# Kernel optimization log

Measured on AMD Instinct MI355X. Metric: run time of the kernel, lower is better.

Reference implementation:

```python
import itertools
import jax, jax.numpy as jnp
import numpy as np

GAMMA = 1.0

def setup_inputs() -> dict:
    key = jax.random.key(0)
    ks = jax.random.split(key, 11)
    B, T, NP, NG, J, H = 16, 32, 8, 4, 14, 256
    return {
        'hor_heatmap': jax.random.normal(ks[0], (B, T, 1, H, H), jnp.float32),
        'hor_offset': jax.random.normal(ks[1], (B, T, NP, 2), jnp.float32),
        'hor_bsize': jax.random.normal(ks[2], (B, T, NP, 4), jnp.float32),
        'hor_center': jax.random.normal(ks[3], (B, T, NP, 2), jnp.float32),
        'scores': jax.random.uniform(ks[4], (B, T, NP), jnp.float32),
        'x_pose3d': jax.random.normal(ks[5], (B, T, NP, J, 3), jnp.float32),
        'gt_heatmap': jax.random.normal(ks[6], (B, T, H, H), jnp.float32),
        'gt_hor_boxes_wh': jax.random.normal(ks[7], (B, T, NG, 4), jnp.float32),
        'gt_hor_offset': jax.random.normal(ks[8], (B, T, NG, 2), jnp.float32),
        'gt_hor_center': jax.random.normal(ks[9], (B, T, NG, 2), jnp.float32),
        'gt_pose3d': jax.random.normal(ks[10], (B, T, NG, J, 3), jnp.float32),
    }

def _make_perms(num_pred, num_gt):
    # all injective assignments of each gt column to a distinct pred row
    return np.asarray(list(itertools.permutations(range(num_pred), num_gt)), dtype=np.int32)

def _match(cost, perms):
    # cost: [NP, NG]; perms: [P, NG] static. Exact linear_sum_assignment by enumeration.
    ng = cost.shape[1]
    totals = cost[perms, jnp.arange(ng)].sum(-1)  # [P]
    return perms[jnp.argmin(totals)]              # rows matched to cols 0..NG-1

def reference(hor_heatmap, hor_offset, hor_bsize, hor_center, scores, x_pose3d,
              gt_heatmap, gt_hor_boxes_wh, gt_hor_offset, gt_hor_center, gt_pose3d):
    B, T, NP, _ = hor_center.shape
    NG = gt_hor_center.shape[2]
    J = x_pose3d.shape[3]
    BT = B * T
    perms = jnp.asarray(_make_perms(NP, NG))

    # center loss: MSE mean over full heatmaps
    center_loss = jnp.mean((hor_heatmap[:, :, 0] - gt_heatmap) ** 2)

    # --- Hungarian box/offset losses, vmapped over (b,t) ---
    def per_bt_box(pc, gc, sc, po, go, ps, gs):
        # cost[i,j] = -score[i] + ||pc_i - gc_j||
        C = jnp.linalg.norm(pc[:, None] - gc[None], axis=-1) - sc[:, None]  # [NP,NG]
        rows = _match(C, perms)                                             # [NG]
        off = jnp.mean(jnp.abs(po[rows] - go), axis=-1).sum()   # L1 mean per pair, summed
        size = jnp.mean(jnp.abs(ps[rows] - gs), axis=-1).sum()
        return off, size

    flat = lambda x: x.reshape((BT,) + x.shape[2:])
    offs, sizes = jax.vmap(per_bt_box)(
        flat(hor_center), flat(gt_hor_center), flat(scores),
        flat(hor_offset), flat(gt_hor_offset), flat(hor_bsize), flat(gt_hor_boxes_wh))
    total_offset_loss = offs.sum() / BT
    total_size_loss = sizes.sum() / BT

    # --- Hungarian pose loss ---
    def per_bt_pose(pp, gp):
        d = pp[:, None] - gp[None]                       # [NP,NG,J,3]
        C = jnp.sqrt(jnp.sum(d * d, axis=(-1, -2)))      # Frobenius norm cost
        rows = _match(C, perms)
        return jnp.sum((pp[rows] - gp) ** 2)             # MSE(sum) per pair, summed

    pose_loss = jax.vmap(per_bt_pose)(flat(x_pose3d), flat(gt_pose3d)).sum() / (BT * NP * J)

    detection_loss = center_loss + total_offset_loss + total_size_loss
    return GAMMA * detection_loss + pose_loss
```

## Files before the change

kernel.cpp:

```cpp
#include <hip/hip_runtime.h>

#define BT      512
#define NP      8
#define NG      4
#define JNT     14
#define NCENTER 33554432
#define N4      8388608
#define CBLK    1024
#define CSTEP   (CBLK*256)
#define HALF4   (N4/2)


__global__ __launch_bounds__(256) void center_kernel(
    const float* __restrict__ hm, const float* __restrict__ gt_hm,
    float* __restrict__ ws, int use_atomics)
{
    __shared__ float sv[4];
    const int tid = threadIdx.x;
    const int base = blockIdx.x * 256 + tid;
    const float4* a = (const float4*)hm;
    const float4* b = (const float4*)gt_hm;
    float s0 = 0.0f, s1 = 0.0f;
    for (int k = 0; k < 16; k++) {
        const int i = base + k * CSTEP;
        float4 x0 = a[i];
        float4 y0 = b[i];
        float4 x1 = a[i + HALF4];
        float4 y1 = b[i + HALF4];
        float d0 = x0.x - y0.x, d1 = x0.y - y0.y, d2 = x0.z - y0.z, d3 = x0.w - y0.w;
        s0 += d0 * d0 + d1 * d1 + d2 * d2 + d3 * d3;
        float e0 = x1.x - y1.x, e1 = x1.y - y1.y, e2 = x1.z - y1.z, e3 = x1.w - y1.w;
        s1 += e0 * e0 + e1 * e1 + e2 * e2 + e3 * e3;
    }
    float s = s0 + s1;
    #pragma unroll
    for (int o = 32; o > 0; o >>= 1) s += __shfl_down(s, o);
    const int lane = tid & 63, w = tid >> 6;
    if (lane == 0) sv[w] = s;
    __syncthreads();
    if (tid == 0) {
        float tot = sv[0] + sv[1] + sv[2] + sv[3];
        if (use_atomics) atomicAdd(&ws[0], tot);
        else             ws[blockIdx.x] = tot;
    }
}

__global__ __launch_bounds__(256) void hungarian_kernel(
    const float* __restrict__ hor_offset,
    const float* __restrict__ hor_bsize,
    const float* __restrict__ hor_center,
    const float* __restrict__ scores,
    const float* __restrict__ x_pose3d,
    const float* __restrict__ gt_wh,
    const float* __restrict__ gt_off,
    const float* __restrict__ gt_center,
    const float* __restrict__ gt_pose,
    float* __restrict__ ws, int use_atomics)
{
    __shared__ float sPP[NP * JNT * 3];
    __shared__ float sGP[NG * JNT * 3];
    __shared__ float sPO[NP * 2];
    __shared__ float sGO[NG * 2];
    __shared__ float sPS[NP * 4];
    __shared__ float sGS[NG * 4];
    __shared__ float sPC[NP * 2];
    __shared__ float sGC[NG * 2];
    __shared__ float sSC[NP];
    __shared__ float2 sCC[NP * NG];
    __shared__ float sv[8];
    __shared__ int   spx[8];
    __shared__ int   sBest[2];

    const int c   = blockIdx.x;
    const int tid = threadIdx.x;

    {
        const float* pp = x_pose3d  + c * (NP * JNT * 3);
        const float* gp = gt_pose   + c * (NG * JNT * 3);
        for (int k = tid; k < NP * JNT * 3; k += 256) sPP[k] = pp[k];
        if (tid < NG * JNT * 3) sGP[tid] = gp[tid];
        if (tid < NP * 2) sPO[tid] = hor_offset[c * NP * 2 + tid];
        if (tid < NG * 2) sGO[tid] = gt_off[c * NG * 2 + tid];
        if (tid < NP * 4) sPS[tid] = hor_bsize[c * NP * 4 + tid];
        if (tid < NG * 4) sGS[tid] = gt_wh[c * NG * 4 + tid];
        if (tid < NP * 2) sPC[tid] = hor_center[c * NP * 2 + tid];
        if (tid < NG * 2) sGC[tid] = gt_center[c * NG * 2 + tid];
        if (tid < NP)     sSC[tid] = scores[c * NP + tid];
    }
    __syncthreads();

    if (tid < 32) {
        const int i = tid >> 2, j = tid & 3;
        float dx = sPC[i * 2 + 0] - sGC[j * 2 + 0];
        float dy = sPC[i * 2 + 1] - sGC[j * 2 + 1];
        float box = sqrtf(dx * dx + dy * dy) - sSC[i];
        float acc = 0.0f;
        #pragma unroll
        for (int k = 0; k < JNT * 3; k++) {
            float d = sPP[i * (JNT * 3) + k] - sGP[j * (JNT * 3) + k];
            acc += d * d;
        }
        sCC[i * 4 + j] = make_float2(box, sqrtf(acc));
    }
    __syncthreads();

    float bv = 1e30f, bv2 = 1e30f;
    int bp = 0x7fffffff, bp2 = 0x7fffffff;
    for (int p = tid; p < 4096; p += 256) {
        const int i0 = (p >> 9) & 7, i1 = (p >> 6) & 7, i2 = (p >> 3) & 7, i3 = p & 7;
        if (i0 == i1 || i0 == i2 || i0 == i3 || i1 == i2 || i1 == i3 || i2 == i3) continue;
        float2 t0 = sCC[i0 * 4 + 0], t1 = sCC[i1 * 4 + 1], t2 = sCC[i2 * 4 + 2], t3 = sCC[i3 * 4 + 3];
        float t  = t0.x + t1.x + t2.x + t3.x;
        float u  = t0.y + t1.y + t2.y + t3.y;
        if (t < bv)  { bv  = t; bp  = p; }
        if (u < bv2) { bv2 = u; bp2 = p; }
    }
    #pragma unroll
    for (int o = 32; o > 0; o >>= 1) {
        float v2 = __shfl_down(bv, o);  int p2 = __shfl_down(bp, o);
        if (v2 < bv  || (v2 == bv  && p2 < bp))  { bv  = v2; bp  = p2; }
        float w2 = __shfl_down(bv2, o); int q2 = __shfl_down(bp2, o);
        if (w2 < bv2 || (w2 == bv2 && q2 < bp2)) { bv2 = w2; bp2 = q2; }
    }
    const int lane = tid & 63, w = tid >> 6;
    if (lane == 0) { sv[w] = bv; spx[w] = bp; sv[4 + w] = bv2; spx[4 + w] = bp2; }
    __syncthreads();
    if (tid == 0) {
        for (int k = 1; k < 4; k++) {
            if (sv[k] < sv[0] || (sv[k] == sv[0] && spx[k] < spx[0])) { sv[0] = sv[k]; spx[0] = spx[k]; }
            if (sv[4 + k] < sv[4] || (sv[4 + k] == sv[4] && spx[4 + k] < spx[4])) { sv[4] = sv[4 + k]; spx[4] = spx[4 + k]; }
        }
        sBest[0] = spx[0];
        sBest[1] = spx[4];
    }
    __syncthreads();

    if (tid < 64) {
        const int pb = sBest[0], pq = sBest[1];
        float contrib = 0.0f;
        if (tid < JNT * 3) {
            float acc = 0.0f;
            #pragma unroll
            for (int jj = 0; jj < 4; jj++) {
                const int r2 = (pq >> (9 - 3 * jj)) & 7;
                float d = sPP[r2 * (JNT * 3) + tid] - sGP[jj * (JNT * 3) + tid];
                acc += d * d;
            }
            contrib += acc * (1.0f / (float)(BT * NP * JNT));
        }
        if (tid < 8) {
            const int jj = tid >> 1, cm = tid & 1;
            const int r = (pb >> (9 - 3 * jj)) & 7;
            contrib += 0.5f * fabsf(sPO[r * 2 + cm] - sGO[jj * 2 + cm]) * (1.0f / (float)BT);
        }
        if (tid < 16) {
            const int jj = tid >> 2, cm = tid & 3;
            const int r = (pb >> (9 - 3 * jj)) & 7;
            contrib += 0.25f * fabsf(sPS[r * 4 + cm] - sGS[jj * 4 + cm]) * (1.0f / (float)BT);
        }
        #pragma unroll
        for (int o = 32; o > 0; o >>= 1) contrib += __shfl_down(contrib, o);
        if (tid == 0) {
            if (use_atomics) atomicAdd(&ws[1], contrib);
            else             ws[CBLK + c] = contrib;
        }
    }
}

__global__ __launch_bounds__(256) void final_partials_kernel(
    const float* __restrict__ ws, float* __restrict__ out)
{
    __shared__ float red[8];
    const int tid = threadIdx.x;
    float s0 = 0.0f, s1 = 0.0f;
    for (int i = tid; i < CBLK; i += 256) s0 += ws[i];
    for (int c = tid; c < BT; c += 256)   s1 += ws[CBLK + c];
    #pragma unroll
    for (int o = 32; o > 0; o >>= 1) {
        s0 += __shfl_down(s0, o);
        s1 += __shfl_down(s1, o);
    }
    const int lane = tid & 63, w = tid >> 6;
    if (lane == 0) { red[w] = s0; red[4 + w] = s1; }
    __syncthreads();
    if (tid == 0) {
        s0 = red[0] + red[1] + red[2] + red[3];
        s1 = red[4] + red[5] + red[6] + red[7];
        out[0] = s0 * (1.0f / (float)NCENTER) + s1;
    }
}

__global__ void init_ws_kernel(float* __restrict__ ws) {
    if (threadIdx.x < 2) ws[threadIdx.x] = 0.0f;
}

__global__ void final_atomic_kernel(const float* __restrict__ ws, float* __restrict__ out) {
    out[0] = ws[0] * (1.0f / (float)NCENTER) + ws[1];
}

extern "C" void kernel_launch(void* const* d_in, const int* in_sizes, int n_in,
                              void* d_out, int out_size, void* d_ws, size_t ws_size,
                              hipStream_t stream) {
    const float* hm         = (const float*)d_in[0];
    const float* hor_offset = (const float*)d_in[1];
    const float* hor_bsize  = (const float*)d_in[2];
    const float* hor_center = (const float*)d_in[3];
    const float* scores     = (const float*)d_in[4];
    const float* x_pose3d   = (const float*)d_in[5];
    const float* gt_hm      = (const float*)d_in[6];
    const float* gt_wh      = (const float*)d_in[7];
    const float* gt_off     = (const float*)d_in[8];
    const float* gt_center  = (const float*)d_in[9];
    const float* gt_pose    = (const float*)d_in[10];
    float* ws  = (float*)d_ws;
    float* out = (float*)d_out;

    const size_t needed = (size_t)(CBLK + BT) * sizeof(float);
    const int use_atomics = (ws_size < needed) ? 1 : 0;

    if (use_atomics) init_ws_kernel<<<1, 64, 0, stream>>>(ws);
    hungarian_kernel<<<BT, 256, 0, stream>>>(
        hor_offset, hor_bsize, hor_center, scores, x_pose3d,
        gt_wh, gt_off, gt_center, gt_pose, ws, use_atomics);
    center_kernel<<<CBLK, 256, 0, stream>>>(hm, gt_hm, ws, use_atomics);
    if (use_atomics) final_atomic_kernel<<<1, 1, 0, stream>>>(ws, out);
    else             final_partials_kernel<<<1, 256, 0, stream>>>(ws, out);
}
```

Baseline: 305.4 us.

## Fuse Hungarian and center-loss kernels into one launch with contiguous per-block tiles

Merges the Hungarian matching kernel and the center MSE reduction into a single kernel, where the first BT blocks do matching and the rest stream the heatmaps. The center part now uses 2048 blocks, each reading a contiguous 4096-float4 chunk with four batched float4 loads per input, instead of 1024 blocks striding across the whole array. The aim is to drop a kernel launch, let the small matching work overlap the bandwidth-bound reduction, and keep more loads in flight. Workspace indexing is reordered to match the new layout.

```diff
diff --git a/kernel.cpp b/kernel.cpp
--- a/kernel.cpp
+++ b/kernel.cpp
@@ -6,51 +6,18 @@
 #define JNT     14
 #define NCENTER 33554432
 #define N4      8388608
-#define CBLK    1024
-#define CSTEP   (CBLK*256)
-#define HALF4   (N4/2)
-
-
-__global__ __launch_bounds__(256) void center_kernel(
-    const float* __restrict__ hm, const float* __restrict__ gt_hm,
-    float* __restrict__ ws, int use_atomics)
-{
-    __shared__ float sv[4];
-    const int tid = threadIdx.x;
-    const int base = blockIdx.x * 256 + tid;
-    const float4* a = (const float4*)hm;
-    const float4* b = (const float4*)gt_hm;
-    float s0 = 0.0f, s1 = 0.0f;
-    for (int k = 0; k < 16; k++) {
-        const int i = base + k * CSTEP;
-        float4 x0 = a[i];
-        float4 y0 = b[i];
-        float4 x1 = a[i + HALF4];
-        float4 y1 = b[i + HALF4];
-        float d0 = x0.x - y0.x, d1 = x0.y - y0.y, d2 = x0.z - y0.z, d3 = x0.w - y0.w;
-        s0 += d0 * d0 + d1 * d1 + d2 * d2 + d3 * d3;
-        float e0 = x1.x - y1.x, e1 = x1.y - y1.y, e2 = x1.z - y1.z, e3 = x1.w - y1.w;
-        s1 += e0 * e0 + e1 * e1 + e2 * e2 + e3 * e3;
-    }
-    float s = s0 + s1;
-    #pragma unroll
-    for (int o = 32; o > 0; o >>= 1) s += __shfl_down(s, o);
-    const int lane = tid & 63, w = tid >> 6;
-    if (lane == 0) sv[w] = s;
-    __syncthreads();
-    if (tid == 0) {
-        float tot = sv[0] + sv[1] + sv[2] + sv[3];
-        if (use_atomics) atomicAdd(&ws[0], tot);
-        else             ws[blockIdx.x] = tot;
-    }
-}
-
-__global__ __launch_bounds__(256) void hungarian_kernel(
+#define CBLK    2048
+#define PER_BLK 4096
+
+
+__global__ __launch_bounds__(256) void fused_kernel(
+    const float* __restrict__ hm,
     const float* __restrict__ hor_offset,
     const float* __restrict__ hor_bsize,
     const float* __restrict__ hor_center,
     const float* __restrict__ scores,
     const float* __restrict__ x_pose3d,
+    const float* __restrict__ gt_hm,
     const float* __restrict__ gt_wh,
     const float* __restrict__ gt_off,
     const float* __restrict__ gt_center,
@@ -71,12 +38,48 @@
     __shared__ int   spx[8];
     __shared__ int   sBest[2];
 
-    const int c   = blockIdx.x;
+    const int blk = blockIdx.x;
     const int tid = threadIdx.x;
 
+    if (blk >= BT) {
+        const int cb = blk - BT;
+        const float4* a = (const float4*)hm;
+        const float4* b = (const float4*)gt_hm;
+        const int base = cb * PER_BLK + tid;
+        float s = 0.0f;
+        #pragma unroll
+        for (int batch = 0; batch < 4; batch++) {
+            float4 xa[4], xb[4];
+            #pragma unroll
+            for (int r = 0; r < 4; r++) xa[r] = a[base + batch * 1024 + r * 256];
+            #pragma unroll
+            for (int r = 0; r < 4; r++) xb[r] = b[base + batch * 1024 + r * 256];
+            #pragma unroll
+            for (int r = 0; r < 4; r++) {
+                float d0 = xa[r].x - xb[r].x;
+                float d1 = xa[r].y - xb[r].y;
+                float d2 = xa[r].z - xb[r].z;
+                float d3 = xa[r].w - xb[r].w;
+                s += d0 * d0 + d1 * d1 + d2 * d2 + d3 * d3;
+            }
+        }
+        #pragma unroll
+        for (int o = 32; o > 0; o >>= 1) s += __shfl_down(s, o);
+        const int lane = tid & 63, w = tid >> 6;
+        if (lane == 0) sv[w] = s;
+        __syncthreads();
+        if (tid == 0) {
+            float tot = sv[0] + sv[1] + sv[2] + sv[3];
+            if (use_atomics) atomicAdd(&ws[0], tot);
+            else             ws[BT + cb] = tot;
+        }
+        return;
+    }
+
+    const int c = blk;
     {
-        const float* pp = x_pose3d  + c * (NP * JNT * 3);
-        const float* gp = gt_pose   + c * (NG * JNT * 3);
+        const float* pp = x_pose3d + c * (NP * JNT * 3);
+        const float* gp = gt_pose  + c * (NG * JNT * 3);
         for (int k = tid; k < NP * JNT * 3; k += 256) sPP[k] = pp[k];
         if (tid < NG * JNT * 3) sGP[tid] = gp[tid];
         if (tid < NP * 2) sPO[tid] = hor_offset[c * NP * 2 + tid];
@@ -110,8 +113,8 @@
         const int i0 = (p >> 9) & 7, i1 = (p >> 6) & 7, i2 = (p >> 3) & 7, i3 = p & 7;
         if (i0 == i1 || i0 == i2 || i0 == i3 || i1 == i2 || i1 == i3 || i2 == i3) continue;
         float2 t0 = sCC[i0 * 4 + 0], t1 = sCC[i1 * 4 + 1], t2 = sCC[i2 * 4 + 2], t3 = sCC[i3 * 4 + 3];
-        float t  = t0.x + t1.x + t2.x + t3.x;
-        float u  = t0.y + t1.y + t2.y + t3.y;
+        float t = t0.x + t1.x + t2.x + t3.x;
+        float u = t0.y + t1.y + t2.y + t3.y;
         if (t < bv)  { bv  = t; bp  = p; }
         if (u < bv2) { bv2 = u; bp2 = p; }
     }
@@ -162,7 +165,7 @@
         for (int o = 32; o > 0; o >>= 1) contrib += __shfl_down(contrib, o);
         if (tid == 0) {
             if (use_atomics) atomicAdd(&ws[1], contrib);
-            else             ws[CBLK + c] = contrib;
+            else             ws[c] = contrib;
         }
     }
 }
@@ -173,8 +176,8 @@
     __shared__ float red[8];
     const int tid = threadIdx.x;
     float s0 = 0.0f, s1 = 0.0f;
-    for (int i = tid; i < CBLK; i += 256) s0 += ws[i];
-    for (int c = tid; c < BT; c += 256)   s1 += ws[CBLK + c];
+    for (int i = tid; i < CBLK; i += 256) s0 += ws[BT + i];
+    for (int c = tid; c < BT; c += 256)   s1 += ws[c];
     #pragma unroll
     for (int o = 32; o > 0; o >>= 1) {
         s0 += __shfl_down(s0, o);
@@ -215,14 +218,13 @@
     float* ws  = (float*)d_ws;
     float* out = (float*)d_out;
 
-    const size_t needed = (size_t)(CBLK + BT) * sizeof(float);
+    const size_t needed = (size_t)(BT + CBLK) * sizeof(float);
     const int use_atomics = (ws_size < needed) ? 1 : 0;
 
     if (use_atomics) init_ws_kernel<<<1, 64, 0, stream>>>(ws);
-    hungarian_kernel<<<BT, 256, 0, stream>>>(
-        hor_offset, hor_bsize, hor_center, scores, x_pose3d,
-        gt_wh, gt_off, gt_center, gt_pose, ws, use_atomics);
-    center_kernel<<<CBLK, 256, 0, stream>>>(hm, gt_hm, ws, use_atomics);
+    fused_kernel<<<BT + CBLK, 256, 0, stream>>>(
+        hm, hor_offset, hor_bsize, hor_center, scores, x_pose3d,
+        gt_hm, gt_wh, gt_off, gt_center, gt_pose, ws, use_atomics);
     if (use_atomics) final_atomic_kernel<<<1, 1, 0, stream>>>(ws, out);
     else             final_partials_kernel<<<1, 256, 0, stream>>>(ws, out);
 }
```

Measured after the change: 297.5 us. 1.03x faster.
